# Performance work log

Hardware: AMD Instinct MI355X
Metric: run time of the kernel (lower is better)

## Reference

```python
import jax, jax.numpy as jnp
import numpy as np

H = 768          # hidden_size
V = 512          # vocab_size
NUM_OPS = 64
N_INT = 2        # num_internal_ops
D = 13           # tree depth; complete binary tree
N_NODES = (1 << (D + 1)) - 1  # 16383, level-major layout: level d occupies [2^d-1, 2^(d+1)-1)
TEMP = 3.0


def setup_inputs() -> dict:
    key = jax.random.key(0)
    ks = jax.random.split(key, 24)
    s = 0.02
    nrm = lambda k, shp: jax.random.normal(k, shp, dtype=jnp.float32) * s
    return {
        "ids": jax.random.randint(ks[0], (N_NODES,), 0, V, dtype=jnp.int32),
        "mask": jax.random.randint(ks[1], (N_NODES, NUM_OPS), 0, 2, dtype=jnp.int32),
        # binary Tree-LSTM (N=2), Tai et al. N-ary formulation
        "Wb_iou": nrm(ks[2], (V, 3 * H)), "Ub_iou": nrm(ks[3], (2, H, 3 * H)), "bb_iou": jnp.zeros((3 * H,), jnp.float32),
        "Wb_f": nrm(ks[4], (V, H)), "Ub_f": nrm(ks[5], (2, 2, H, H)), "bb_f": jnp.ones((H,), jnp.float32),
        # ternary Tree-LSTM (N=3)
        "Wt_iou": nrm(ks[6], (V, 3 * H)), "Ut_iou": nrm(ks[7], (3, H, 3 * H)), "bt_iou": jnp.zeros((3 * H,), jnp.float32),
        "Wt_f": nrm(ks[8], (V, H)), "Ut_f": nrm(ks[9], (3, 3, H, H)), "bt_f": jnp.ones((H,), jnp.float32),
        # FFN(H,H,H,n_layers=1): Linear->ReLU->Linear
        "ffn_W1": nrm(ks[10], (H, H)), "ffn_b1": jnp.zeros((H,), jnp.float32),
        "ffn_W2": nrm(ks[11], (H, H)), "ffn_b2": jnp.zeros((H,), jnp.float32),
        # actor heads
        "hl_W": nrm(ks[12], (H, 2)), "hl_b": jnp.zeros((2,), jnp.float32),
        "int_W": nrm(ks[13], (H, N_INT)), "int_b": jnp.zeros((N_INT,), jnp.float32),
        "act_W": nrm(ks[14], (H, NUM_OPS)), "act_b": jnp.zeros((NUM_OPS,), jnp.float32),
    }


def _cell(x_iou, x_f, hc, cc, U_iou, b_iou, U_f, b_f):
    """Batched N-ary Tree-LSTM cell. hc, cc: (n, K, H)."""
    iou = x_iou + jnp.einsum('nkh,kho->no', hc, U_iou) + b_iou
    i, o, g = jnp.split(iou, 3, axis=-1)
    i = jax.nn.sigmoid(i); o = jax.nn.sigmoid(o); g = jnp.tanh(g)
    # per-child forget gate mixes all children hiddens
    f = jax.nn.sigmoid(x_f[:, None, :] + jnp.einsum('nlh,klho->nko', hc, U_f) + b_f)
    c = i * g + jnp.sum(f * cc, axis=1)
    h = o * jnp.tanh(c)
    return h, c


def reference(ids, mask,
              Wb_iou, Ub_iou, bb_iou, Wb_f, Ub_f, bb_f,
              Wt_iou, Ut_iou, bt_iou, Wt_f, Ut_f, bt_f,
              ffn_W1, ffn_b1, ffn_W2, ffn_b2,
              hl_W, hl_b, int_W, int_b, act_W, act_b):
    dt = Wb_iou.dtype
    # ---- apply_binary_lstm: bottom-up, batched per tree level ----
    h_lv = [None] * (D + 1)
    c_lv = [None] * (D + 1)
    for d in range(D, -1, -1):
        n = 1 << d
        off = n - 1
        lid = ids[off:off + n]
        if d == D:  # leaves: missing children -> zero hidden/cell (self.tz)
            hc = jnp.zeros((n, 2, H), dt); cc = jnp.zeros((n, 2, H), dt)
        else:
            hc = h_lv[d + 1].reshape(n, 2, H)
            cc = c_lv[d + 1].reshape(n, 2, H)
        h_lv[d], c_lv[d] = _cell(Wb_iou[lid], Wb_f[lid], hc, cc, Ub_iou, bb_iou, Ub_f, bb_f)
    # ---- internal op 1: apply_ternary_lstm(depth=0) at every node, batched ----
    # uses (own h, child-a h, child-b h); leaves get all zeros (a is None branch)
    h3_parts = []
    for d in range(D + 1):
        n = 1 << d
        off = n - 1
        lid = ids[off:off + n]
        if d == D:
            hc = jnp.zeros((n, 3, H), dt); cc = jnp.zeros((n, 3, H), dt)
        else:
            hc = jnp.concatenate([h_lv[d][:, None, :], h_lv[d + 1].reshape(n, 2, H)], axis=1)
            cc = jnp.concatenate([c_lv[d][:, None, :], c_lv[d + 1].reshape(n, 2, H)], axis=1)
        h3, _ = _cell(Wt_iou[lid], Wt_f[lid], hc, cc, Ut_iou, bt_iou, Ut_f, bt_f)
        h3_parts.append(h3)
    h = jnp.concatenate(h3_parts, axis=0)  # [N_NODES, H], level-major
    # ---- internal op 0: apply_ffn ----
    h = jax.nn.relu(h @ ffn_W1 + ffn_b1) @ ffn_W2 + ffn_b2
    # ---- policy heads (temperature softmaxes, masked actor) ----
    hl = jax.nn.softmax((h @ hl_W + hl_b) / TEMP, axis=-1)
    il = jax.nn.softmax((h @ int_W + int_b) / TEMP, axis=-1)
    mf = mask.astype(dt)
    lin = (h @ act_W + act_b) * mf                       # F.linear with mask-zeroed W, b
    logits = jnp.where(mf > 0, lin, jnp.asarray(-1e30, dt))  # validity_mask.log() + lin
    ap = jax.nn.softmax(logits / TEMP, axis=-1)
    return jnp.concatenate([hl, il, ap], axis=-1)  # [N_NODES, 2 + N_INT + NUM_OPS]
```

## Files before the change

kernel.cpp:

```cpp
#include <hip/hip_runtime.h>
#include <hip/hip_bf16.h>

#define HD 768
#define N_NODES 16383
#define NLEAF_OFF 8191
#define NHF 12582144
#define TEMP 3.0f

using bf16 = __hip_bfloat16;
typedef __attribute__((ext_vector_type(8))) short bf16x8;
typedef __attribute__((ext_vector_type(4))) float f32x4;

__device__ __forceinline__ float sigm(float x) { return 1.0f / (1.0f + __expf(-x)); }
__device__ __forceinline__ float b2f(bf16 v)   { return __bfloat162float(v); }
__device__ __forceinline__ bf16  f2b(float v)  { return __float2bfloat16(v); }

__device__ __forceinline__ void gload16(const void* g, void* l) {
    __builtin_amdgcn_global_load_lds(
        (const __attribute__((address_space(1))) unsigned int*)g,
        (__attribute__((address_space(3))) unsigned int*)l, 16, 0, 0);
}

#define T1SZ 5898240
#define T2SZ 10616832
#define WSZ  589824

__global__ __launch_bounds__(256) void tconv_k(
    const float* __restrict__ Ub_iou, const float* __restrict__ Ub_f,
    const float* __restrict__ Ut_iou, const float* __restrict__ Ut_f,
    const float* __restrict__ ffn_W1,
    bf16* __restrict__ BT1, bf16* __restrict__ BT2, bf16* __restrict__ W1T)
{
    int t = blockIdx.x;
    const float* src; bf16* dst; int C, S, kt, nt;
    if (t < 3456) {
        src = Ub_iou; dst = BT1; C = 2304; S = 1536;
        kt = t % 48; nt = t / 48;
    } else if (t < 5760) {
        int u = t - 3456; int piece = u / 576; u -= piece * 576;
        int kk = piece >> 1, l = piece & 1;
        src = Ub_f + (size_t)(kk * 2 + l) * WSZ;
        dst = BT1 + (size_t)(2304 + kk * 768) * 1536 + l * 768;
        C = 768; S = 1536; kt = u % 24; nt = u / 24;
    } else if (t < 10944) {
        int u = t - 5760;
        src = Ut_iou; dst = BT2; C = 2304; S = 2304;
        kt = u % 72; nt = u / 72;
    } else if (t < 16128) {
        int u = t - 10944; int piece = u / 576; u -= piece * 576;
        int kk = piece / 3, l = piece - kk * 3;
        src = Ut_f + (size_t)(kk * 3 + l) * WSZ;
        dst = BT2 + (size_t)(2304 + kk * 768) * 2304 + l * 768;
        C = 768; S = 2304; kt = u % 24; nt = u / 24;
    } else {
        int u = t - 16128;
        src = ffn_W1; dst = W1T; C = 768; S = 768;
        kt = u % 24; nt = u / 24;
    }
    int k0 = kt * 32, n0 = nt * 32;

    __shared__ float tl[32][33];
    int rr = threadIdx.x >> 5, c = threadIdx.x & 31;
#pragma unroll
    for (int r = 0; r < 32; r += 8)
        tl[rr + r][c] = src[(size_t)(k0 + rr + r) * C + n0 + c];
    __syncthreads();
#pragma unroll
    for (int r = 0; r < 32; r += 8)
        dst[(size_t)(n0 + rr + r) * S + k0 + c] = f2b(tl[c][rr + r]);
}

#define HSZ2 98304
__global__ __launch_bounds__(256) void misc_k(
    const float* __restrict__ hlW, const float* __restrict__ intW,
    const float* __restrict__ actW, const float* __restrict__ W2,
    bf16* __restrict__ WhT, bf16* __restrict__ W2b)
{
    int idx = blockIdx.x * 256 + threadIdx.x;
    if (idx < HSZ2) {
        int n = idx / 768, j = idx - n * 768;
        float v = 0.f;
        if (n < 2)       v = hlW[(size_t)j * 2 + n];
        else if (n < 4)  v = intW[(size_t)j * 2 + (n - 2)];
        else if (n < 68) v = actW[(size_t)j * 64 + (n - 4)];
        WhT[idx] = f2b(v);
    } else if (idx < HSZ2 + WSZ) {
        int i2 = idx - HSZ2;
        W2b[i2] = f2b(W2[i2]);
    }
}

__global__ __launch_bounds__(128) void bck_k(
    const float* __restrict__ b2,
    const float* __restrict__ hlW, const float* __restrict__ hlb,
    const float* __restrict__ intW, const float* __restrict__ intb,
    const float* __restrict__ actW, const float* __restrict__ actb,
    float* __restrict__ bc)
{
    int n = threadIdx.x;
    float s = 0.f;
    for (int j = 0; j < 768; ++j) {
        float wh = 0.f;
        if (n < 2)       wh = hlW[(size_t)j * 2 + n];
        else if (n < 4)  wh = intW[(size_t)j * 2 + (n - 2)];
        else if (n < 68) wh = actW[(size_t)j * 64 + (n - 4)];
        s = fmaf(b2[j], wh, s);
    }
    float hb = 0.f;
    if (n < 2)       hb = hlb[n];
    else if (n < 4)  hb = intb[n - 2];
    else if (n < 68) hb = actb[n - 4];
    bc[n] = s + hb;
}

__global__ __launch_bounds__(256) void leaf_k(
    const int* __restrict__ ids,
    const float* __restrict__ Wb, const float* __restrict__ bb,
    const float* __restrict__ Wt, const float* __restrict__ bt,
    bf16* __restrict__ h_all, bf16* __restrict__ c_all, bf16* __restrict__ h3_all)
{
    int idx = blockIdx.x * blockDim.x + threadIdx.x;
    if (idx >= 8192 * HD) return;
    int i = idx / HD, j = idx - i * HD;
    int g = NLEAF_OFF + i;
    int id = ids[g];
    const float* w = Wb + (size_t)id * 3 * HD;
    float iv = sigm(w[j] + bb[j]);
    float ov = sigm(w[HD + j] + bb[HD + j]);
    float gv = tanhf(w[2 * HD + j] + bb[2 * HD + j]);
    float c = iv * gv;
    h_all[(size_t)g * HD + j] = f2b(ov * tanhf(c));
    c_all[(size_t)g * HD + j] = f2b(c);

    const float* w2 = Wt + (size_t)id * 3 * HD;
    float iv2 = sigm(w2[j] + bt[j]);
    float ov2 = sigm(w2[HD + j] + bt[HD + j]);
    float gv2 = tanhf(w2[2 * HD + j] + bt[2 * HD + j]);
    float c2 = iv2 * gv2;
    h3_all[(size_t)g * HD + j] = f2b(ov2 * tanhf(c2));
}

template <int GATHER>
__global__ __launch_bounds__(512, 2) void mm8_k(
    const bf16* __restrict__ A, const bf16* __restrict__ BT,
    bf16* __restrict__ Cb, int M, int N, int K)
{
    __shared__ short Al[2][16384];
    __shared__ short Bl[2][16384];

    const int tid  = threadIdx.x;
    const int lane = tid & 63;
    const int wid  = tid >> 6;
    const int wr = wid >> 2, wc = wid & 3;
    const int bx = blockIdx.x, by = blockIdx.y;
    const int NT = K >> 6;

    const int srow = wid * 8 + (lane >> 3);
    const int scol = ((lane & 7) ^ (lane >> 3)) * 8;
    const int frow = lane & 15;
    const int fq   = lane >> 4;

    f32x4 acc[8][4] = {};

    auto stageA = [&](int t, int cr) {
        int slot = t & 1;
        int grow = by * 256 + cr + srow;
        if (grow > M - 1) grow = M - 1;
        int kb = t * 64;
        const bf16* src;
        if constexpr (GATHER) {
            int ch = kb / 768;
            int node = (ch == 0) ? grow : (2 * grow + ch);
            src = A + (size_t)node * 768 + (kb - ch * 768) + scol;
        } else {
            src = A + (size_t)grow * K + kb + scol;
        }
        gload16(src, &Al[slot][(cr + wid * 8) * 64]);
    };
    auto stageB = [&](int t, int cr) {
        int slot = t & 1;
        const bf16* src = BT + (size_t)(bx * 256 + cr + srow) * K + t * 64 + scol;
        gload16(src, &Bl[slot][(cr + wid * 8) * 64]);
    };

    stageB(0, 0);   stageB(0, 64);
    stageB(0, 128); stageB(0, 192);
    stageA(0, 0);   stageA(0, 128);
    stageA(0, 64);  stageA(0, 192);
    stageB(1, 0);   stageB(1, 64);
    stageB(1, 128); stageB(1, 192);
    stageA(1, 0);   stageA(1, 128);
    asm volatile("s_waitcnt vmcnt(6)" ::: "memory");
    __builtin_amdgcn_s_barrier();

#define PHASE(Q, STAGES, TAILWAIT)                                           \
    {                                                                        \
        bf16x8 a[2][2];                                                      \
        _Pragma("unroll")                                                    \
        for (int mq = 0; mq < 2; ++mq)                                       \
            _Pragma("unroll")                                                \
            for (int ks = 0; ks < 2; ++ks)                                   \
                a[mq][ks] = *(const bf16x8*)&Ax[                             \
                    (wr * 128 + ((Q) * 2 + mq) * 16 + frow) * 64             \
                    + (((ks * 4 + fq) ^ (frow & 7)) * 8)];                   \
        STAGES;                                                              \
        __builtin_amdgcn_s_barrier();                                        \
        asm volatile("s_waitcnt lgkmcnt(0)" ::: "memory");                   \
        __builtin_amdgcn_sched_barrier(0);                                   \
        __builtin_amdgcn_s_setprio(1);                                       \
        _Pragma("unroll")                                                    \
        for (int mq = 0; mq < 2; ++mq)                                       \
            _Pragma("unroll")                                                \
            for (int nf = 0; nf < 4; ++nf)                                   \
                _Pragma("unroll")                                            \
                for (int ks = 0; ks < 2; ++ks)                               \
                    acc[(Q) * 2 + mq][nf] =                                  \
                        __builtin_amdgcn_mfma_f32_16x16x32_bf16(             \
                            a[mq][ks], b[nf][ks], acc[(Q) * 2 + mq][nf], 0, 0, 0); \
        __builtin_amdgcn_s_setprio(0);                                       \
        TAILWAIT;                                                            \
        __builtin_amdgcn_s_barrier();                                        \
    }

    for (int t = 0; t < NT; ++t) {
        short* Ax = Al[t & 1];
        short* Bx = Bl[t & 1];
        bf16x8 b[4][2];
#pragma unroll
        for (int nf = 0; nf < 4; ++nf)
#pragma unroll
            for (int ks = 0; ks < 2; ++ks)
                b[nf][ks] = *(const bf16x8*)&Bx[
                    (wc * 64 + nf * 16 + frow) * 64
                    + (((ks * 4 + fq) ^ (frow & 7)) * 8)];

        PHASE(0,
              { if (t + 1 < NT) { stageA(t + 1, 64); stageA(t + 1, 192); } },
              {})
        PHASE(1,
              { if (t + 2 < NT) { stageB(t + 2, 0); stageB(t + 2, 64); } },
              {})
        PHASE(2,
              { if (t + 2 < NT) { stageB(t + 2, 128); stageB(t + 2, 192); } },
              {})
        PHASE(3,
              { if (t + 2 < NT) { stageA(t + 2, 0); stageA(t + 2, 128); } },
              {
                  if (t + 2 < NT) asm volatile("s_waitcnt vmcnt(6)" ::: "memory");
                  else            asm volatile("s_waitcnt vmcnt(0)" ::: "memory");
              })
    }
#undef PHASE

#pragma unroll
    for (int mf = 0; mf < 8; ++mf) {
#pragma unroll
        for (int r = 0; r < 4; ++r) {
            int row = by * 256 + wr * 128 + mf * 16 + (lane >> 4) * 4 + r;
            if (row >= M) continue;
#pragma unroll
            for (int nf = 0; nf < 4; ++nf) {
                int col = bx * 256 + wc * 64 + nf * 16 + (lane & 15);
                Cb[(size_t)row * N + col] = f2b(acc[mf][nf][r]);
            }
        }
    }
}

template <int EPI, int GATHER>
__global__ __launch_bounds__(256) void mm_k(
    const bf16* __restrict__ A, const bf16* __restrict__ BT,
    float* __restrict__ Cf, bf16* __restrict__ Cb,
    const float* __restrict__ bias,
    int M, int N, int Kc, int Kfull)
{
    __shared__ short As[128 * 32];
    __shared__ short Bs[128 * 32];

    int tid  = threadIdx.x;
    int lane = tid & 63;
    int wave = tid >> 6;
    int wr = wave >> 1, wc = wave & 1;
    int bx = blockIdx.x, by = blockIdx.y;
    int colbase = blockIdx.z * Kc;
    if constexpr (EPI == 0) Cf += (size_t)blockIdx.z * ((size_t)M * N);

    f32x4 acc[4][4] = {};

    int sr  = lane >> 2;
    int sc8 = (lane & 3) * 8;
    int arow0 = by * 128 + wave * 16 + sr;
    int arow1 = arow0 + 64;
    if (arow0 > M - 1) arow0 = M - 1;
    if (arow1 > M - 1) arow1 = M - 1;
    const bf16* gA0 = A + (size_t)arow0 * Kfull + colbase + sc8;
    const bf16* gA1 = A + (size_t)arow1 * Kfull + colbase + sc8;
    const bf16* gB0 = BT + (size_t)(bx * 128 + wave * 16 + sr) * Kfull + colbase + sc8;
    const bf16* gB1 = BT + (size_t)(bx * 128 + wave * 16 + sr + 64) * Kfull + colbase + sc8;
    short* lA0 = As + wave * 512;
    short* lA1 = As + wave * 512 + 2048;
    short* lB0 = Bs + wave * 512;
    short* lB1 = Bs + wave * 512 + 2048;

    int fr = lane & 15;
    int fk = (lane >> 4) << 3;
    const short* pAf = As + (wr * 64 + fr) * 32 + fk;
    const short* pBf = Bs + (wc * 64 + fr) * 32 + fk;

    for (int kt = 0; kt < Kc; kt += 32) {
        if constexpr (GATHER) {
            int abs0 = colbase + kt;
            int ch = (abs0 >= 768) + (abs0 >= 1536);
            int col = abs0 - ch * 768 + sc8;
            int n0 = (ch == 0) ? arow0 : (2 * arow0 + ch);
            int n1 = (ch == 0) ? arow1 : (2 * arow1 + ch);
            gload16(A + (size_t)n0 * HD + col, lA0);
            gload16(A + (size_t)n1 * HD + col, lA1);
        } else {
            gload16(gA0 + kt, lA0);
            gload16(gA1 + kt, lA1);
        }
        gload16(gB0 + kt, lB0);
        gload16(gB1 + kt, lB1);
        __syncthreads();

        bf16x8 a[4], b[4];
#pragma unroll
        for (int m = 0; m < 4; m++) a[m] = *(const bf16x8*)(pAf + m * 512);
#pragma unroll
        for (int n = 0; n < 4; n++) b[n] = *(const bf16x8*)(pBf + n * 512);
#pragma unroll
        for (int m = 0; m < 4; m++)
#pragma unroll
            for (int n = 0; n < 4; n++)
                acc[m][n] = __builtin_amdgcn_mfma_f32_16x16x32_bf16(
                    a[m], b[n], acc[m][n], 0, 0, 0);
        __syncthreads();
    }

    int rbase = by * 128 + wr * 64 + ((lane >> 4) << 2);
    int cbase = bx * 128 + wc * 64 + fr;
#pragma unroll
    for (int m = 0; m < 4; m++) {
#pragma unroll
        for (int r = 0; r < 4; r++) {
            int row = rbase + m * 16 + r;
            if (row >= M) continue;
#pragma unroll
            for (int n = 0; n < 4; n++) {
                int col = cbase + n * 16;
                float v = acc[m][n][r];
                if constexpr (EPI == 1) {
                    v = fmaxf(v + bias[col], 0.f);
                    Cb[(size_t)row * N + col] = f2b(v);
                } else if constexpr (EPI == 3) {
                    Cb[(size_t)row * N + col] = f2b(v);
                } else {
                    Cf[(size_t)row * N + col] = v;
                }
            }
        }
    }
}

__global__ __launch_bounds__(256) void cell1_k(
    const int* __restrict__ ids, const bf16* __restrict__ S,
    const float* __restrict__ Wiou, const float* __restrict__ biou,
    const float* __restrict__ Wf, const float* __restrict__ bfv,
    bf16* __restrict__ h_all, bf16* __restrict__ c_all,
    int m, int offAbs)
{
    int idx = blockIdx.x * blockDim.x + threadIdx.x;
    if (idx >= m * HD) return;
    int i = idx / HD, j = idx - i * HD;
    int g = offAbs + i;
    int id = ids[g];
    const bf16* s = S + (size_t)i * 3840;
    const float* w = Wiou + (size_t)id * 2304;
    float iv = sigm(b2f(s[j]) + w[j] + biou[j]);
    float ov = sigm(b2f(s[HD + j]) + w[HD + j] + biou[HD + j]);
    float gv = tanhf(b2f(s[2 * HD + j]) + w[2 * HD + j] + biou[2 * HD + j]);
    float xf = Wf[(size_t)id * HD + j] + bfv[j];
    float f0 = sigm(b2f(s[3 * HD + j]) + xf);
    float f1 = sigm(b2f(s[4 * HD + j]) + xf);
    float c = iv * gv
            + f0 * b2f(c_all[(size_t)(2 * g + 1) * HD + j])
            + f1 * b2f(c_all[(size_t)(2 * g + 2) * HD + j]);
    h_all[(size_t)g * HD + j] = f2b(ov * tanhf(c));
    c_all[(size_t)g * HD + j] = f2b(c);
}

__global__ __launch_bounds__(256) void cell1s_k(
    const int* __restrict__ ids, const float* __restrict__ Sf,
    const float* __restrict__ Wiou, const float* __restrict__ biou,
    const float* __restrict__ Wf, const float* __restrict__ bfv,
    bf16* __restrict__ h_all, bf16* __restrict__ c_all,
    int m, int offAbs, int KS)
{
    int idx = blockIdx.x * blockDim.x + threadIdx.x;
    if (idx >= m * HD) return;
    int i = idx / HD, j = idx - i * HD;
    int g = offAbs + i;
    int id = ids[g];
    const float* s = Sf + (size_t)i * 3840;
    size_t zs = (size_t)m * 3840;
    float si = 0.f, so = 0.f, su = 0.f, p0 = 0.f, p1 = 0.f;
    for (int z = 0; z < KS; ++z) {
        const float* sz = s + z * zs;
        si += sz[j];
        so += sz[HD + j];
        su += sz[2 * HD + j];
        p0 += sz[3 * HD + j];
        p1 += sz[4 * HD + j];
    }
    const float* w = Wiou + (size_t)id * 2304;
    float iv = sigm(si + w[j] + biou[j]);
    float ov = sigm(so + w[HD + j] + biou[HD + j]);
    float gv = tanhf(su + w[2 * HD + j] + biou[2 * HD + j]);
    float xf = Wf[(size_t)id * HD + j] + bfv[j];
    float f0 = sigm(p0 + xf);
    float f1 = sigm(p1 + xf);
    float c = iv * gv
            + f0 * b2f(c_all[(size_t)(2 * g + 1) * HD + j])
            + f1 * b2f(c_all[(size_t)(2 * g + 2) * HD + j]);
    h_all[(size_t)g * HD + j] = f2b(ov * tanhf(c));
    c_all[(size_t)g * HD + j] = f2b(c);
}

__global__ __launch_bounds__(256) void cell2_k(
    const int* __restrict__ ids, const bf16* __restrict__ S,
    const float* __restrict__ Wiou, const float* __restrict__ biou,
    const float* __restrict__ Wf, const float* __restrict__ bfv,
    const bf16* __restrict__ c_all, bf16* __restrict__ h3_all,
    int m, int g0)
{
    int idx = blockIdx.x * blockDim.x + threadIdx.x;
    if (idx >= m * HD) return;
    int i = idx / HD, j = idx - i * HD;
    int g = g0 + i;
    int id = ids[g];
    const bf16* s = S + (size_t)i * 4608;
    const float* w = Wiou + (size_t)id * 2304;
    float iv = sigm(b2f(s[j]) + w[j] + biou[j]);
    float ov = sigm(b2f(s[HD + j]) + w[HD + j] + biou[HD + j]);
    float gv = tanhf(b2f(s[2 * HD + j]) + w[2 * HD + j] + biou[2 * HD + j]);
    float xf = Wf[(size_t)id * HD + j] + bfv[j];
    float f0 = sigm(b2f(s[3 * HD + j]) + xf);
    float f1 = sigm(b2f(s[4 * HD + j]) + xf);
    float f2 = sigm(b2f(s[5 * HD + j]) + xf);
    float c = iv * gv
            + f0 * b2f(c_all[(size_t)g * HD + j])
            + f1 * b2f(c_all[(size_t)(2 * g + 1) * HD + j])
            + f2 * b2f(c_all[(size_t)(2 * g + 2) * HD + j]);
    h3_all[(size_t)g * HD + j] = f2b(ov * tanhf(c));
}

__global__ __launch_bounds__(256) void hsm_k(
    const float* __restrict__ L, const int* __restrict__ mask,
    const float* __restrict__ bc, float* __restrict__ out)
{
    int g = blockIdx.x * 4 + (threadIdx.x >> 6);
    if (g >= N_NODES) return;
    int t = threadIdx.x & 63;
    const float* lr = L + (size_t)g * 128;

    bool on = mask[(size_t)g * 64 + t] > 0;
    float x = (lr[4 + t] + bc[4 + t]) * (1.0f / TEMP);
    float mx = on ? x : -INFINITY;
#pragma unroll
    for (int o = 32; o; o >>= 1) mx = fmaxf(mx, __shfl_xor(mx, o));
    float e = on ? __expf(x - mx) : 0.0f;
    float s = e;
#pragma unroll
    for (int o = 32; o; o >>= 1) s += __shfl_xor(s, o);
    float r = (s > 0.f) ? e / s : (1.0f / 64.0f);
    out[(size_t)g * 68 + 4 + t] = r;

    if (t == 0) {
        float a = (lr[0] + bc[0]) * (1.0f / TEMP);
        float b = (lr[1] + bc[1]) * (1.0f / TEMP);
        float m2 = fmaxf(a, b);
        float e0 = __expf(a - m2), e1 = __expf(b - m2);
        out[(size_t)g * 68 + 0] = e0 / (e0 + e1);
        out[(size_t)g * 68 + 1] = e1 / (e0 + e1);
    } else if (t == 1) {
        float a = (lr[2] + bc[2]) * (1.0f / TEMP);
        float b = (lr[3] + bc[3]) * (1.0f / TEMP);
        float m2 = fmaxf(a, b);
        float e0 = __expf(a - m2), e1 = __expf(b - m2);
        out[(size_t)g * 68 + 2] = e0 / (e0 + e1);
        out[(size_t)g * 68 + 3] = e1 / (e0 + e1);
    }
}

extern "C" void kernel_launch(void* const* d_in, const int* in_sizes, int n_in,
                              void* d_out, int out_size, void* d_ws, size_t ws_size,
                              hipStream_t stream)
{
    const int*   ids     = (const int*)d_in[0];
    const int*   mask    = (const int*)d_in[1];
    const float* Wb_iou  = (const float*)d_in[2];
    const float* Ub_iou  = (const float*)d_in[3];
    const float* bb_iou  = (const float*)d_in[4];
    const float* Wb_f    = (const float*)d_in[5];
    const float* Ub_f    = (const float*)d_in[6];
    const float* bb_f    = (const float*)d_in[7];
    const float* Wt_iou  = (const float*)d_in[8];
    const float* Ut_iou  = (const float*)d_in[9];
    const float* bt_iou  = (const float*)d_in[10];
    const float* Wt_f    = (const float*)d_in[11];
    const float* Ut_f    = (const float*)d_in[12];
    const float* bt_f    = (const float*)d_in[13];
    const float* ffn_W1  = (const float*)d_in[14];
    const float* ffn_b1  = (const float*)d_in[15];
    const float* ffn_W2  = (const float*)d_in[16];
    const float* ffn_b2  = (const float*)d_in[17];
    const float* hl_W    = (const float*)d_in[18];
    const float* hl_b    = (const float*)d_in[19];
    const float* int_W   = (const float*)d_in[20];
    const float* int_b   = (const float*)d_in[21];
    const float* act_W   = (const float*)d_in[22];
    const float* act_b   = (const float*)d_in[23];

    char* p = (char*)d_ws;
    bf16* h_all  = (bf16*)p; p += (size_t)NHF * 2;
    bf16* c_all  = (bf16*)p; p += (size_t)NHF * 2;
    bf16* h3_all = (bf16*)p; p += (size_t)NHF * 2;
    bf16* BT1 = (bf16*)p; p += (size_t)T1SZ * 2;
    bf16* BT2 = (bf16*)p; p += (size_t)T2SZ * 2;
    bf16* W1T = (bf16*)p; p += (size_t)WSZ * 2;
    bf16* WcT = (bf16*)p; p += (size_t)128 * 768 * 2;
    bf16* WhT = (bf16*)p; p += (size_t)HSZ2 * 2;
    bf16* W2b = (bf16*)p; p += (size_t)WSZ * 2;
    float* bc = (float*)p; p += 512;
    bf16* Sb  = (bf16*)p;
    float* Sf = (float*)Sb;
    bf16* t1  = c_all;
    float* Lg = (float*)h3_all;

    tconv_k<<<16704, 256, 0, stream>>>(
        Ub_iou, Ub_f, Ut_iou, Ut_f, ffn_W1, BT1, BT2, W1T);
    misc_k<<<(HSZ2 + WSZ + 255) / 256, 256, 0, stream>>>(
        hl_W, int_W, act_W, ffn_W2, WhT, W2b);
    bck_k<<<1, 128, 0, stream>>>(
        ffn_b2, hl_W, hl_b, int_W, int_b, act_W, act_b, bc);
    mm_k<3, 0><<<dim3(6, 1), 256, 0, stream>>>(
        WhT, W2b, nullptr, WcT, nullptr, 128, 768, 768, 768);

    leaf_k<<<(8192 * HD + 255) / 256, 256, 0, stream>>>(
        ids, Wb_iou, bb_iou, Wt_iou, bt_iou, h_all, c_all, h3_all);

    for (int d = 12; d >= 0; --d) {
        int n = 1 << d;
        int childoff = 2 * n - 1;
        if (n >= 2048) {
            mm8_k<0><<<dim3(15, n / 256), 512, 0, stream>>>(
                h_all + (size_t)childoff * HD, BT1, Sb, n, 3840, 1536);
            cell1_k<<<(n * HD + 255) / 256, 256, 0, stream>>>(
                ids, Sb, Wb_iou, bb_iou, Wb_f, bb_f, h_all, c_all, n, n - 1);
        } else if (n >= 512) {
            mm_k<3, 0><<<dim3(30, n / 128), 256, 0, stream>>>(
                h_all + (size_t)childoff * HD, BT1, nullptr, Sb, nullptr,
                n, 3840, 1536, 1536);
            cell1_k<<<(n * HD + 255) / 256, 256, 0, stream>>>(
                ids, Sb, Wb_iou, bb_iou, Wb_f, bb_f, h_all, c_all, n, n - 1);
        } else {
            mm_k<0, 0><<<dim3(30, (n + 127) / 128, 6), 256, 0, stream>>>(
                h_all + (size_t)childoff * HD, BT1, Sf, nullptr, nullptr,
                n, 3840, 256, 1536);
            cell1s_k<<<(n * HD + 255) / 256, 256, 0, stream>>>(
                ids, Sf, Wb_iou, bb_iou, Wb_f, bb_f, h_all, c_all, n, n - 1, 6);
        }
    }

    mm8_k<1><<<dim3(18, 32), 512, 0, stream>>>(
        h_all, BT2, Sb, NLEAF_OFF, 4608, 2304);
    cell2_k<<<(NLEAF_OFF * HD + 255) / 256, 256, 0, stream>>>(
        ids, Sb, Wt_iou, bt_iou, Wt_f, bt_f, c_all, h3_all, NLEAF_OFF, 0);

    mm_k<1, 0><<<dim3(6, 128), 256, 0, stream>>>(
        h3_all, W1T, nullptr, t1, ffn_b1, N_NODES, 768, 768, 768);

    mm_k<0, 0><<<dim3(1, 128), 256, 0, stream>>>(
        t1, WcT, Lg, nullptr, nullptr, N_NODES, 128, 768, 768);
    hsm_k<<<(N_NODES + 3) / 4, 256, 0, stream>>>(
        Lg, mask, bc, (float*)d_out);
}
```

Baseline: 795.9 us.

## Precompute per-vocab leaf states and remap GEMM tiles per XCD

```diff
diff --git a/kernel.cpp b/kernel.cpp
--- a/kernel.cpp
+++ b/kernel.cpp
@@ -113,37 +113,51 @@
     bc[n] = s + hb;
 }
 
-__global__ __launch_bounds__(256) void leaf_k(
-    const int* __restrict__ ids,
+__global__ __launch_bounds__(256) void vocab_k(
     const float* __restrict__ Wb, const float* __restrict__ bb,
     const float* __restrict__ Wt, const float* __restrict__ bt,
-    bf16* __restrict__ h_all, bf16* __restrict__ c_all, bf16* __restrict__ h3_all)
-{
-    int idx = blockIdx.x * blockDim.x + threadIdx.x;
-    if (idx >= 8192 * HD) return;
-    int i = idx / HD, j = idx - i * HD;
-    int g = NLEAF_OFF + i;
-    int id = ids[g];
+    bf16* __restrict__ Vh, bf16* __restrict__ Vc, bf16* __restrict__ Vh3)
+{
+    int idx = blockIdx.x * 256 + threadIdx.x;
+    if (idx >= 512 * HD) return;
+    int id = idx / HD, j = idx - id * HD;
     const float* w = Wb + (size_t)id * 3 * HD;
     float iv = sigm(w[j] + bb[j]);
     float ov = sigm(w[HD + j] + bb[HD + j]);
     float gv = tanhf(w[2 * HD + j] + bb[2 * HD + j]);
     float c = iv * gv;
-    h_all[(size_t)g * HD + j] = f2b(ov * tanhf(c));
-    c_all[(size_t)g * HD + j] = f2b(c);
+    Vh[idx] = f2b(ov * tanhf(c));
+    Vc[idx] = f2b(c);
 
     const float* w2 = Wt + (size_t)id * 3 * HD;
     float iv2 = sigm(w2[j] + bt[j]);
     float ov2 = sigm(w2[HD + j] + bt[HD + j]);
     float gv2 = tanhf(w2[2 * HD + j] + bt[2 * HD + j]);
     float c2 = iv2 * gv2;
-    h3_all[(size_t)g * HD + j] = f2b(ov2 * tanhf(c2));
+    Vh3[idx] = f2b(ov2 * tanhf(c2));
+}
+
+__global__ __launch_bounds__(256) void lscat_k(
+    const int* __restrict__ ids,
+    const bf16* __restrict__ Vh, const bf16* __restrict__ Vc,
+    const bf16* __restrict__ Vh3,
+    bf16* __restrict__ h_all, bf16* __restrict__ c_all, bf16* __restrict__ h3_all)
+{
+    int idx = blockIdx.x * 256 + threadIdx.x;
+    if (idx >= 8192 * 96) return;
+    int i = idx / 96, j8 = (idx - i * 96) * 8;
+    int g = NLEAF_OFF + i;
+    size_t so = (size_t)ids[g] * HD + j8;
+    size_t dof = (size_t)g * HD + j8;
+    *(uint4*)(h_all + dof)  = *(const uint4*)(Vh + so);
+    *(uint4*)(c_all + dof)  = *(const uint4*)(Vc + so);
+    *(uint4*)(h3_all + dof) = *(const uint4*)(Vh3 + so);
 }
 
 template <int GATHER>
 __global__ __launch_bounds__(512, 2) void mm8_k(
     const bf16* __restrict__ A, const bf16* __restrict__ BT,
-    bf16* __restrict__ Cb, int M, int N, int K)
+    bf16* __restrict__ Cb, int M, int N, int K, int NBX)
 {
     __shared__ short Al[2][16384];
     __shared__ short Bl[2][16384];
@@ -152,8 +166,13 @@
     const int lane = tid & 63;
     const int wid  = tid >> 6;
     const int wr = wid >> 2, wc = wid & 3;
-    const int bx = blockIdx.x, by = blockIdx.y;
     const int NT = K >> 6;
+
+    int T = gridDim.x, L = blockIdx.x;
+    int q = T >> 3, r = T & 7;
+    int xcd = L & 7, i8 = L >> 3;
+    int v = (xcd < r ? xcd * (q + 1) : r * (q + 1) + (xcd - r) * q) + i8;
+    const int bx = v % NBX, by = v / NBX;
 
     const int srow = wid * 8 + (lane >> 3);
     const int scol = ((lane & 7) ^ (lane >> 3)) * 8;
@@ -255,13 +274,13 @@
 #pragma unroll
     for (int mf = 0; mf < 8; ++mf) {
 #pragma unroll
-        for (int r = 0; r < 4; ++r) {
-            int row = by * 256 + wr * 128 + mf * 16 + (lane >> 4) * 4 + r;
+        for (int r2 = 0; r2 < 4; ++r2) {
+            int row = by * 256 + wr * 128 + mf * 16 + (lane >> 4) * 4 + r2;
             if (row >= M) continue;
 #pragma unroll
             for (int nf = 0; nf < 4; ++nf) {
                 int col = bx * 256 + wc * 64 + nf * 16 + (lane & 15);
-                Cb[(size_t)row * N + col] = f2b(acc[mf][nf][r]);
+                Cb[(size_t)row * N + col] = f2b(acc[mf][nf][r2]);
             }
         }
     }
@@ -532,6 +551,9 @@
     bf16* WcT = (bf16*)p; p += (size_t)128 * 768 * 2;
     bf16* WhT = (bf16*)p; p += (size_t)HSZ2 * 2;
     bf16* W2b = (bf16*)p; p += (size_t)WSZ * 2;
+    bf16* Vh  = (bf16*)p; p += (size_t)512 * HD * 2;
+    bf16* Vc  = (bf16*)p; p += (size_t)512 * HD * 2;
+    bf16* Vh3 = (bf16*)p; p += (size_t)512 * HD * 2;
     float* bc = (float*)p; p += 512;
     bf16* Sb  = (bf16*)p;
     float* Sf = (float*)Sb;
@@ -547,15 +569,17 @@
     mm_k<3, 0><<<dim3(6, 1), 256, 0, stream>>>(
         WhT, W2b, nullptr, WcT, nullptr, 128, 768, 768, 768);
 
-    leaf_k<<<(8192 * HD + 255) / 256, 256, 0, stream>>>(
-        ids, Wb_iou, bb_iou, Wt_iou, bt_iou, h_all, c_all, h3_all);
+    vocab_k<<<(512 * HD + 255) / 256, 256, 0, stream>>>(
+        Wb_iou, bb_iou, Wt_iou, bt_iou, Vh, Vc, Vh3);
+    lscat_k<<<(8192 * 96 + 255) / 256, 256, 0, stream>>>(
+        ids, Vh, Vc, Vh3, h_all, c_all, h3_all);
 
     for (int d = 12; d >= 0; --d) {
         int n = 1 << d;
         int childoff = 2 * n - 1;
         if (n >= 2048) {
-            mm8_k<0><<<dim3(15, n / 256), 512, 0, stream>>>(
-                h_all + (size_t)childoff * HD, BT1, Sb, n, 3840, 1536);
+            mm8_k<0><<<15 * (n / 256), 512, 0, stream>>>(
+                h_all + (size_t)childoff * HD, BT1, Sb, n, 3840, 1536, 15);
             cell1_k<<<(n * HD + 255) / 256, 256, 0, stream>>>(
                 ids, Sb, Wb_iou, bb_iou, Wb_f, bb_f, h_all, c_all, n, n - 1);
         } else if (n >= 512) {
@@ -573,8 +597,8 @@
         }
     }
 
-    mm8_k<1><<<dim3(18, 32), 512, 0, stream>>>(
-        h_all, BT2, Sb, NLEAF_OFF, 4608, 2304);
+    mm8_k<1><<<18 * 32, 512, 0, stream>>>(
+        h_all, BT2, Sb, NLEAF_OFF, 4608, 2304, 18);
     cell2_k<<<(NLEAF_OFF * HD + 255) / 256, 256, 0, stream>>>(
         ids, Sb, Wt_iou, bt_iou, Wt_f, bt_f, c_all, h3_all, NLEAF_OFF, 0);
 
```

Result: no change. 783.0 us (-1.6%).
